# Kernel tuning notes

Measured on AMD Instinct MI355X. Metric: run time of the kernel, lower is better.

The kernel has to match this reference:

```python
import jax, jax.numpy as jnp
import numpy as np


def _scan_dir(x, A, B, reverse):
    """First-order linear recurrence h_i = A*h_{i-1} + B*x_i along last axis (W).
    x: [Bsz, C, H, W]; A, B: [C]. reverse=True scans right-to-left but returns
    states in original index order (matching torch scan_backward)."""
    xs = jnp.moveaxis(x, -1, 0)  # [W, Bsz, C, H]
    Ab = A[None, :, None]
    Bb = B[None, :, None]
    def step(h, xi):
        h = Ab * h + Bb * xi
        return h, h
    h0 = jnp.zeros_like(xs[0])
    _, hs = jax.lax.scan(step, h0, xs, reverse=reverse)
    return jnp.moveaxis(hs, 0, -1)  # [Bsz, C, H, W]


def _conv1x1(x, W, b):
    # x: [B,Cin,H,W], W: [Cout,Cin], b: [Cout]
    return jnp.einsum('bchw,dc->bdhw', x, W) + b[None, :, None, None]


def setup_inputs() -> dict:
    key = jax.random.key(0)
    ks = jax.random.split(key, 10)
    B, C, H, W = 8, 64, 128, 128
    D = 128  # hidden_dim
    return {
        'F_in': jax.random.normal(ks[0], (B, C, H, W), dtype=jnp.float32),
        'prior': jax.random.uniform(ks[1], (B, 1, H, W), dtype=jnp.float32),
        'Wi': jax.random.normal(ks[2], (D, C), dtype=jnp.float32) * 0.05,
        'bi': jnp.zeros((D,), dtype=jnp.float32),
        'A_param': jax.random.normal(ks[3], (D,), dtype=jnp.float32),
        'B_param': jax.random.normal(ks[4], (D,), dtype=jnp.float32),
        'alpha': jnp.float32(0.1),
        'gamma': jnp.float32(0.1),
        'Wf': jax.random.normal(ks[5], (D, 4 * D), dtype=jnp.float32) * 0.05,
        'bf': jnp.zeros((D,), dtype=jnp.float32),
        'Wo': jax.random.normal(ks[6], (C, D), dtype=jnp.float32) * 0.05,
        'bo': jnp.zeros((C,), dtype=jnp.float32),
    }


def reference(F_in, prior, Wi, bi, A_param, B_param, alpha, gamma, Wf, bf, Wo, bo):
    # prior has 1 channel, repeated to C channels (prior already matches HxW)
    prior_r = jnp.broadcast_to(prior, F_in.shape)
    F_mod = F_in + alpha * prior_r
    x = _conv1x1(F_mod, Wi, bi)  # [B, D, H, W]
    A = jnp.tanh(A_param)
    Bp = B_param
    h_lr = _scan_dir(x, A, Bp, reverse=False)
    h_rl = _scan_dir(x, A, Bp, reverse=True)
    xt = jnp.swapaxes(x, 2, 3)  # scan over H axis
    h_tb = jnp.swapaxes(_scan_dir(xt, A, Bp, reverse=False), 2, 3)
    h_bt = jnp.swapaxes(_scan_dir(xt, A, Bp, reverse=True), 2, 3)
    h = jnp.concatenate([h_lr, h_rl, h_tb, h_bt], axis=1)  # [B, 4D, H, W]
    h = _conv1x1(h, Wf, bf)   # fusion -> [B, D, H, W]
    out = _conv1x1(h, Wo, bo)  # output_proj -> [B, C, H, W]
    return F_mod + gamma * out
```

## Files before the change

kernel.cpp:

```cpp
#include <hip/hip_runtime.h>
#include <hip/hip_bf16.h>

typedef unsigned int u32;
typedef unsigned short u16;
typedef float f32x2 __attribute__((ext_vector_type(2)));
typedef float f32x4 __attribute__((ext_vector_type(4)));
using bf16x8 = __attribute__((ext_vector_type(8))) short;
using f32x4v = __attribute__((ext_vector_type(4))) float;

#define DEVINL __device__ __forceinline__

constexpr int LDS_AB = 65536;
constexpr int XS = 132;
constexpr int LDS_X = 128 * XS * 2;

DEVINL float bf2f(u16 u) { union { u32 i; float f; } v; v.i = ((u32)u) << 16; return v.f; }
DEVINL float bf2f_lo(u32 u) { union { u32 i; float f; } v; v.i = u << 16; return v.f; }
DEVINL float bf2f_hi(u32 u) { union { u32 i; float f; } v; v.i = u & 0xffff0000u; return v.f; }
DEVINL u16 f2bf(float f) {
  __hip_bfloat16 h = __float2bfloat16(f);
  u16 r; __builtin_memcpy(&r, &h, 2); return r;
}
DEVINL u32 pack2(float a, float b) { return (u32)f2bf(a) | ((u32)f2bf(b) << 16); }

__global__ __launch_bounds__(256) void k_pre(
    const float* __restrict__ Wf, const float* __restrict__ Wo,
    const float* __restrict__ bf_, const float* __restrict__ bo,
    const float* __restrict__ A_param, const float* __restrict__ Wi,
    float* __restrict__ A_t, float* __restrict__ beff,
    u16* __restrict__ Mrow, u16* __restrict__ Wi_bf) {
  const int wg = blockIdx.x, t = threadIdx.x;
  if (wg < 128) {
    const int idx = wg * 256 + t;
    const int cout = idx >> 9;
    const int k = idx & 511;
    float s = 0.f;
    for (int d = 0; d < 128; ++d) s = fmaf(Wo[cout * 128 + d], Wf[d * 512 + k], s);
    const int dir = k >> 7, dm = k & 127;
    Mrow[(dir * 64 + cout) * 128 + dm] = f2bf(s);
  } else if (wg == 128) {
    if (t < 128) A_t[t] = tanhf(A_param[t]);
    if (t < 64) {
      float s = bo[t];
      for (int d = 0; d < 128; ++d) s = fmaf(Wo[t * 128 + d], bf_[d], s);
      beff[t] = s;
    }
  } else {
#pragma unroll
    for (int k = 0; k < 32; ++k) {
      const int i = t + k * 256;
      Wi_bf[i] = f2bf(Wi[i]);
    }
  }
}

extern __shared__ char smem[];

template <bool REV>
DEVINL void scan_local(char* buf, int dp, int chunk, f32x2 A2) {
  f32x2 h = { 0.f, 0.f };
  const u32 cb = (u32)(dp * 4);
  const int s = chunk * 32;
  u32 nx[8];
#pragma unroll
  for (int j = 0; j < 8; ++j) {
    const int i = REV ? (127 - (s + j)) : (s + j);
    nx[j] = *(const u32*)(buf + i * 256 + (cb ^ ((u32)((i & 7) << 4))));
  }
  for (int ib = 0; ib < 32; ib += 8) {
    u32 cur[8];
#pragma unroll
    for (int j = 0; j < 8; ++j) cur[j] = nx[j];
    if (ib + 8 < 32) {
#pragma unroll
      for (int j = 0; j < 8; ++j) {
        const int i2 = s + ib + 8 + j;
        const int i = REV ? (127 - i2) : i2;
        nx[j] = *(const u32*)(buf + i * 256 + (cb ^ ((u32)((i & 7) << 4))));
      }
    }
#pragma unroll
    for (int j = 0; j < 8; ++j) {
      const int i2 = s + ib + j;
      const int i = REV ? (127 - i2) : i2;
      const f32x2 xv = { bf2f_lo(cur[j]), bf2f_hi(cur[j]) };
      h = A2 * h + xv;
      *(u32*)(buf + i * 256 + (cb ^ ((u32)((i & 7) << 4)))) = pack2(h.x, h.y);
    }
  }
}

template <bool REV>
DEVINL void scan_fix(char* buf, int dp, int chunk, f32x2 A2) {
  if (chunk == 0) return;
  f32x2 q = A2;
#pragma unroll
  for (int k = 0; k < 5; ++k) q *= q;
  const u32 cb = (u32)(dp * 4);
  f32x2 C = { 0.f, 0.f };
  for (int k = 0; k < chunk; ++k) {
    const int i2 = k * 32 + 31;
    const int i = REV ? (127 - i2) : i2;
    const u32 v = *(const u32*)(buf + i * 256 + (cb ^ ((u32)((i & 7) << 4))));
    const f32x2 xv = { bf2f_lo(v), bf2f_hi(v) };
    C = C * q + xv;
  }
  f32x2 p = A2;
  const int s = chunk * 32;
  u32 nx[8];
#pragma unroll
  for (int j = 0; j < 8; ++j) {
    const int i = REV ? (127 - (s + j)) : (s + j);
    nx[j] = *(const u32*)(buf + i * 256 + (cb ^ ((u32)((i & 7) << 4))));
  }
  for (int ib = 0; ib < 32; ib += 8) {
    u32 cur[8];
#pragma unroll
    for (int j = 0; j < 8; ++j) cur[j] = nx[j];
    if (ib + 8 < 32) {
#pragma unroll
      for (int j = 0; j < 8; ++j) {
        const int i2 = s + ib + 8 + j;
        const int i = REV ? (127 - i2) : i2;
        nx[j] = *(const u32*)(buf + i * 256 + (cb ^ ((u32)((i & 7) << 4))));
      }
    }
#pragma unroll
    for (int j = 0; j < 8; ++j) {
      const int i2 = s + ib + j;
      const int i = REV ? (127 - i2) : i2;
      const f32x2 xv = { bf2f_lo(cur[j]), bf2f_hi(cur[j]) };
      const f32x2 hv = p * C + xv;
      *(u32*)(buf + i * 256 + (cb ^ ((u32)((i & 7) << 4)))) = pack2(hv.x, hv.y);
      p *= A2;
    }
  }
}

DEVINL void run_scans512(char* bufA, char* bufB, int t, const float* __restrict__ A_t) {
  const int sub = t & 255, dp = sub & 63, chunk = sub >> 6, dir = t >> 8;
  const f32x2 a = *(const f32x2*)(A_t + dp * 2);
  char* sb = dir ? bufB : bufA;
  if (dir == 0) scan_local<false>(sb, dp, chunk, a);
  else          scan_local<true >(sb, dp, chunk, a);
  __syncthreads();
  if (dir == 0) scan_fix<false>(sb, dp, chunk, a);
  else          scan_fix<true >(sb, dp, chunk, a);
}

DEVINL void combine_full(const char* bufA, const char* bufB, const u16* __restrict__ Mrow,
                         int dir_base, int eh, int wq, int l15, int kg,
                         f32x4v (&acc2)[2][2]) {
#pragma unroll
  for (int dir = 0; dir < 2; ++dir) {
    const char* buf = dir ? bufB : bufA;
#pragma unroll
    for (int ks = 0; ks < 4; ++ks) {
      bf16x8 afr[2], bfr[2];
#pragma unroll
      for (int ct = 0; ct < 2; ++ct)
        afr[ct] = *(const bf16x8*)(Mrow + ((size_t)(dir_base + dir) * 64 + eh * 32 + ct * 16 + l15) * 128 + ks * 32 + kg * 8);
#pragma unroll
      for (int pt = 0; pt < 2; ++pt) {
        const int row = wq * 32 + pt * 16 + l15;
        bfr[pt] = *(const bf16x8*)(buf + row * 256 + ((u32)(ks * 64 + kg * 16) ^ ((u32)((row & 7) << 4))));
      }
#pragma unroll
      for (int ct = 0; ct < 2; ++ct)
#pragma unroll
        for (int pt = 0; pt < 2; ++pt)
          acc2[ct][pt] = __builtin_amdgcn_mfma_f32_16x16x32_bf16(bfr[pt], afr[ct], acc2[ct][pt], 0, 0, 0);
    }
  }
}

DEVINL void outs_epilogue512(const f32x4v (&acc2)[2][2], int eh, int wq, int l15, int kg,
                             int t, u16* __restrict__ og) {
#pragma unroll
  for (int ct = 0; ct < 2; ++ct)
#pragma unroll
    for (int pt = 0; pt < 2; ++pt) {
      const int c = eh * 32 + ct * 16 + l15;
      const int pos = wq * 32 + pt * 16 + kg * 4;
      *(f32x4v*)(smem + c * 512 + ((u32)(pos * 4) ^ ((u32)((c & 7) << 4)))) = acc2[ct][pt];
    }
  __syncthreads();
#pragma unroll
  for (int j = 0; j < 8; ++j) {
    const int i = t + j * 512;
    const int c = i >> 6, p2 = (i & 63) * 2;
    const f32x2 v = *(const f32x2*)(smem + c * 512 + ((u32)(p2 * 4) ^ ((u32)((c & 7) << 4))));
    *(u32*)(og + c * 128 + p2) = pack2(v.x, v.y);
  }
}

__global__ __launch_bounds__(512, 4) void k_A(
    const float* __restrict__ F_in, const float* __restrict__ prior,
    const u16* __restrict__ Wi_bf, const float* __restrict__ bi,
    const float* __restrict__ Bp, const float* __restrict__ alpha_p,
    const float* __restrict__ A_t, const u16* __restrict__ Mrow,
    u16* __restrict__ x2, u16* __restrict__ Shp) {
  char* bufA = smem;
  char* bufB = smem + 32768;

  const int t = threadIdx.x;
  const int lane = t & 63, wv = t >> 6;
  const int l15 = lane & 15, kg = lane >> 4;
  const int bid = blockIdx.x, b = bid >> 7, h = bid & 127;
  const int wq = wv & 3, eh = wv >> 2;

  {
    const int w = t & 127, ch = t >> 7;
    const float alpha = alpha_p[0];
    const float pv = prior[(b * 128 + h) * 128 + w];
    const float* Fb = F_in + ((size_t)b * 64 + ch * 16) * 16384 + h * 128 + w;
    const u32 sw = ((u32)((w & 7) << 4)) | (((u32)(w >> 3) & 1u) << 7);
    char* rowp = bufA + w * 256;
#pragma unroll
    for (int q = 0; q < 2; ++q) {
      float fv[8];
#pragma unroll
      for (int j = 0; j < 8; ++j) fv[j] = fmaf(alpha, pv, Fb[(q * 8 + j) * 16384]);
      uint4 pk;
      pk.x = pack2(fv[0], fv[1]); pk.y = pack2(fv[2], fv[3]);
      pk.z = pack2(fv[4], fv[5]); pk.w = pack2(fv[6], fv[7]);
      *(uint4*)(rowp + ((u32)(ch * 32 + q * 16) ^ sw)) = pk;
    }
  }
  __syncthreads();

  bf16x8 bF[2][2];
#pragma unroll
  for (int wj = 0; wj < 2; ++wj)
#pragma unroll
    for (int ks = 0; ks < 2; ++ks) {
      const int row = wq * 32 + wj * 16 + l15;
      const u32 sw = ((u32)((row & 7) << 4)) | (((u32)(row >> 3) & 1u) << 7);
      bF[wj][ks] = *(const bf16x8*)(bufA + row * 256 + ((u32)(ks * 64 + kg * 16) ^ sw));
    }
  __syncthreads();

  {
    f32x4v acc[4][2];
#pragma unroll
    for (int dt = 0; dt < 4; ++dt) {
      const f32x4 bv = *(const f32x4*)(bi + eh * 64 + dt * 16 + kg * 4);
      const f32x4v bvv = { bv.x, bv.y, bv.z, bv.w };
#pragma unroll
      for (int wj = 0; wj < 2; ++wj) acc[dt][wj] = bvv;
    }
#pragma unroll
    for (int ks = 0; ks < 2; ++ks)
#pragma unroll
      for (int dt = 0; dt < 4; ++dt) {
        const bf16x8 aWi = *(const bf16x8*)(Wi_bf + (eh * 64 + dt * 16 + l15) * 64 + ks * 32 + kg * 8);
        acc[dt][0] = __builtin_amdgcn_mfma_f32_16x16x32_bf16(aWi, bF[0][ks], acc[dt][0], 0, 0, 0);
        acc[dt][1] = __builtin_amdgcn_mfma_f32_16x16x32_bf16(aWi, bF[1][ks], acc[dt][1], 0, 0, 0);
      }
#pragma unroll
    for (int dt = 0; dt < 4; ++dt) {
      const f32x4 B4 = *(const f32x4*)(Bp + eh * 64 + dt * 16 + kg * 4);
      const f32x4v B4v = { B4.x, B4.y, B4.z, B4.w };
#pragma unroll
      for (int wj = 0; wj < 2; ++wj) {
        const f32x4v sv = acc[dt][wj] * B4v;
        const int w = wq * 32 + wj * 16 + l15;
        const int dl = eh * 64 + dt * 16 + kg * 4;
        uint2 pk;
        pk.x = pack2(sv[0], sv[1]);
        pk.y = pack2(sv[2], sv[3]);
        const u32 col = (u32)(dl * 2) ^ ((u32)((w & 7) << 4));
        *(uint2*)(bufA + w * 256 + col) = pk;
        *(uint2*)(bufB + w * 256 + col) = pk;
      }
    }
  }
  __syncthreads();

  {
    u16* xg = x2 + (size_t)bid * 16384;
#pragma unroll
    for (int j = 0; j < 4; ++j) {
      const int idx = t + j * 512;
      const int row = idx >> 4, q = idx & 15;
      const uint4 v = *(const uint4*)(bufA + row * 256 + ((u32)(q * 16) ^ ((u32)((row & 7) << 4))));
      *(uint4*)(xg + row * 128 + q * 8) = v;
    }
  }
  __syncthreads();

  run_scans512(bufA, bufB, t, A_t);
  __syncthreads();

  f32x4v acc2[2][2];
#pragma unroll
  for (int i = 0; i < 2; ++i)
#pragma unroll
    for (int j = 0; j < 2; ++j) acc2[i][j] = (f32x4v)0.f;
  combine_full(bufA, bufB, Mrow, 0, eh, wq, l15, kg, acc2);
  __syncthreads();
  outs_epilogue512(acc2, eh, wq, l15, kg, t, Shp + (size_t)bid * 8192);
}

__global__ __launch_bounds__(512, 4) void k_B(
    const u16* __restrict__ x2,
    const float* __restrict__ A_t, const u16* __restrict__ Mrow,
    u16* __restrict__ Svp) {
  char* bufA = smem;
  char* bufB = smem + 32768;

  const int t = threadIdx.x;
  const int lane = t & 63, wv = t >> 6;
  const int l15 = lane & 15, kg = lane >> 4;
  const int bid = blockIdx.x, b = bid >> 7, w = bid & 127;
  const int wq = wv & 3, eh = wv >> 2;

#pragma unroll
  for (int j = 0; j < 4; ++j) {
    const int idx = t + j * 512;
    const int hh = idx >> 4, q = idx & 15;
    const uint4 v = *(const uint4*)(x2 + ((size_t)(b * 128 + hh) * 128 + w) * 128 + q * 8);
    const u32 col = (u32)(q * 16) ^ ((u32)((hh & 7) << 4));
    *(uint4*)(bufA + hh * 256 + col) = v;
    *(uint4*)(bufB + hh * 256 + col) = v;
  }
  __syncthreads();

  run_scans512(bufA, bufB, t, A_t);
  __syncthreads();

  f32x4v acc2[2][2];
#pragma unroll
  for (int i = 0; i < 2; ++i)
#pragma unroll
    for (int j = 0; j < 2; ++j) acc2[i][j] = (f32x4v)0.f;
  combine_full(bufA, bufB, Mrow, 2, eh, wq, l15, kg, acc2);
  __syncthreads();
  outs_epilogue512(acc2, eh, wq, l15, kg, t, Svp + (size_t)bid * 8192);
}

__global__ __launch_bounds__(256) void k_final(
    const float* __restrict__ F_in, const float* __restrict__ prior,
    const float* __restrict__ alpha_p, const float* __restrict__ gamma_p,
    const float* __restrict__ beff, const u16* __restrict__ Svp,
    const u16* __restrict__ Shp, float* __restrict__ out) {
  u16* Xu = (u16*)smem;
  const int t = threadIdx.x;
  const int bid = blockIdx.x, b = bid >> 6, c = bid & 63;
  const size_t base = (size_t)bid * 16384;

  for (int i = t; i < 2048; i += 256) {
    const int w = i >> 4, q = i & 15;
    const uint4 a4 = *(const uint4*)(Svp + (size_t)(b * 128 + w) * 8192 + c * 128 + q * 8);
    u32* dst = (u32*)(Xu + w * 132 + q * 8);
    dst[0] = a4.x; dst[1] = a4.y; dst[2] = a4.z; dst[3] = a4.w;
  }
  __syncthreads();
  const float alpha = alpha_p[0], gamma = gamma_p[0];
  const float be = beff[c];
  for (int i = t; i < 2048; i += 256) {
    const int hh = i >> 4, w8 = (i & 15) * 8;
    const size_t off = base + hh * 128 + w8;
    const uint4 g0 = *(const uint4*)(Shp + (size_t)(b * 128 + hh) * 8192 + c * 128 + w8);
    const u16* p0 = (const u16*)&g0;
    const float* Fp = F_in + off;
    float* Op = out + off;
    const float* Pp = prior + (b * 128 + hh) * 128 + w8;
#pragma unroll
    for (int q = 0; q < 8; ++q) {
      const float sv = bf2f(Xu[(w8 + q) * 132 + hh]);
      Op[q] = Fp[q] + alpha * Pp[q] + gamma * (bf2f(p0[q]) + sv + be);
    }
  }
}

extern "C" void kernel_launch(void* const* d_in, const int* in_sizes, int n_in,
                              void* d_out, int out_size, void* d_ws, size_t ws_size,
                              hipStream_t stream) {
  const float* F_in   = (const float*)d_in[0];
  const float* prior  = (const float*)d_in[1];
  const float* Wi     = (const float*)d_in[2];
  const float* bi     = (const float*)d_in[3];
  const float* A_par  = (const float*)d_in[4];
  const float* B_par  = (const float*)d_in[5];
  const float* alpha  = (const float*)d_in[6];
  const float* gamma  = (const float*)d_in[7];
  const float* Wf     = (const float*)d_in[8];
  const float* bf_    = (const float*)d_in[9];
  const float* Wo     = (const float*)d_in[10];
  const float* bo     = (const float*)d_in[11];
  float* out = (float*)d_out;

  char* ws = (char*)d_ws;
  float* A_t   = (float*)ws;
  float* beff  = (float*)(ws + 512);
  u16*   Mrow  = (u16*)(ws + 1024);
  u16*   Wi_bf = (u16*)(ws + 66560);
  u16*   x2    = (u16*)(ws + 82944);
  u16*   Shp   = (u16*)(ws + 82944 + 33554432);
  u16*   Svp   = (u16*)(ws + 82944 + 67108864);

  hipFuncSetAttribute((const void*)k_A, hipFuncAttributeMaxDynamicSharedMemorySize, LDS_AB);
  hipFuncSetAttribute((const void*)k_B, hipFuncAttributeMaxDynamicSharedMemorySize, LDS_AB);

  k_pre  <<<130, 256, 0, stream>>>(Wf, Wo, bf_, bo, A_par, Wi, A_t, beff, Mrow, Wi_bf);
  k_A    <<<1024, 512, LDS_AB, stream>>>(F_in, prior, Wi_bf, bi, B_par, alpha, A_t, Mrow, x2, Shp);
  k_B    <<<1024, 512, LDS_AB, stream>>>(x2, A_t, Mrow, Svp);
  k_final<<<512, 256, LDS_X, stream>>>(F_in, prior, alpha, gamma, beff, Svp, Shp, out);
}
```

Measured before the change: 94.98 us.

## Reuse a single LDS buffer for forward and reverse scans to halve shared memory

Each scan/combine kernel previously kept two 32 KB LDS copies so the forward and backward scans could run at the same time on 512 threads. It now keeps one buffer. The forward scan runs first and its combine MFMA is applied. The forward states are then turned back into reverse-scan states in place, using a local recurrence plus a boundary value, and the second combine runs. This halves LDS per block, which should let more blocks fit per CU. The cost is that the two directions now run one after the other with only half the threads active, extra barriers are added, and the extra bf16 rounding may reduce accuracy.

```diff
diff --git a/kernel.cpp b/kernel.cpp
--- a/kernel.cpp
+++ b/kernel.cpp
@@ -10,7 +10,7 @@
 
 #define DEVINL __device__ __forceinline__
 
-constexpr int LDS_AB = 65536;
+constexpr int LDS_AB = 32768;
 constexpr int XS = 132;
 constexpr int LDS_X = 128 * XS * 2;
 
@@ -137,41 +137,95 @@
   }
 }
 
-DEVINL void run_scans512(char* bufA, char* bufB, int t, const float* __restrict__ A_t) {
-  const int sub = t & 255, dp = sub & 63, chunk = sub >> 6, dir = t >> 8;
-  const f32x2 a = *(const f32x2*)(A_t + dp * 2);
-  char* sb = dir ? bufB : bufA;
-  if (dir == 0) scan_local<false>(sb, dp, chunk, a);
-  else          scan_local<true >(sb, dp, chunk, a);
-  __syncthreads();
-  if (dir == 0) scan_fix<false>(sb, dp, chunk, a);
-  else          scan_fix<true >(sb, dp, chunk, a);
-}
-
-DEVINL void combine_full(const char* bufA, const char* bufB, const u16* __restrict__ Mrow,
-                         int dir_base, int eh, int wq, int l15, int kg,
-                         f32x4v (&acc2)[2][2]) {
-#pragma unroll
-  for (int dir = 0; dir < 2; ++dir) {
-    const char* buf = dir ? bufB : bufA;
-#pragma unroll
-    for (int ks = 0; ks < 4; ++ks) {
-      bf16x8 afr[2], bfr[2];
-#pragma unroll
-      for (int ct = 0; ct < 2; ++ct)
-        afr[ct] = *(const bf16x8*)(Mrow + ((size_t)(dir_base + dir) * 64 + eh * 32 + ct * 16 + l15) * 128 + ks * 32 + kg * 8);
-#pragma unroll
-      for (int pt = 0; pt < 2; ++pt) {
-        const int row = wq * 32 + pt * 16 + l15;
-        bfr[pt] = *(const bf16x8*)(buf + row * 256 + ((u32)(ks * 64 + kg * 16) ^ ((u32)((row & 7) << 4))));
+DEVINL void rev_convert(char* buf, int dp, int chunk, f32x2 A2, f32x2 bnd) {
+  const u32 cb = (u32)(dp * 4);
+  const int s = chunk * 32;
+  f32x2 h = { 0.f, 0.f };
+  u32 nx[8];
+#pragma unroll
+  for (int j = 0; j < 8; ++j) {
+    const int i = 127 - (s + j);
+    nx[j] = *(const u32*)(buf + i * 256 + (cb ^ ((u32)((i & 7) << 4))));
+  }
+  for (int ib = 0; ib < 32; ib += 8) {
+    u32 cur[8];
+#pragma unroll
+    for (int j = 0; j < 8; ++j) cur[j] = nx[j];
+    const bool more = (ib + 8 < 32);
+    if (more) {
+#pragma unroll
+      for (int j = 0; j < 8; ++j) {
+        const int i = 127 - (s + ib + 8 + j);
+        nx[j] = *(const u32*)(buf + i * 256 + (cb ^ ((u32)((i & 7) << 4))));
       }
-#pragma unroll
-      for (int ct = 0; ct < 2; ++ct)
-#pragma unroll
-        for (int pt = 0; pt < 2; ++pt)
-          acc2[ct][pt] = __builtin_amdgcn_mfma_f32_16x16x32_bf16(bfr[pt], afr[ct], acc2[ct][pt], 0, 0, 0);
-    }
-  }
+    }
+#pragma unroll
+    for (int j = 0; j < 8; ++j) {
+      const int i2 = s + ib + j;
+      const int i = 127 - i2;
+      const f32x2 hc = { bf2f_lo(cur[j]), bf2f_hi(cur[j]) };
+      f32x2 hn;
+      if (j < 7)     hn = (f32x2){ bf2f_lo(cur[j + 1]), bf2f_hi(cur[j + 1]) };
+      else if (more) hn = (f32x2){ bf2f_lo(nx[0]), bf2f_hi(nx[0]) };
+      else           hn = bnd;
+      const f32x2 bx = hc - A2 * hn;
+      h = A2 * h + bx;
+      *(u32*)(buf + i * 256 + (cb ^ ((u32)((i & 7) << 4)))) = pack2(h.x, h.y);
+    }
+  }
+}
+
+DEVINL void combine_one(const char* buf, const u16* __restrict__ Mrow, int dirIdx,
+                        int eh, int wq, int l15, int kg, f32x4v (&acc2)[2][2]) {
+#pragma unroll
+  for (int ks = 0; ks < 4; ++ks) {
+    bf16x8 afr[2], bfr[2];
+#pragma unroll
+    for (int ct = 0; ct < 2; ++ct)
+      afr[ct] = *(const bf16x8*)(Mrow + ((size_t)dirIdx * 64 + eh * 32 + ct * 16 + l15) * 128 + ks * 32 + kg * 8);
+#pragma unroll
+    for (int pt = 0; pt < 2; ++pt) {
+      const int row = wq * 32 + pt * 16 + l15;
+      bfr[pt] = *(const bf16x8*)(buf + row * 256 + ((u32)(ks * 64 + kg * 16) ^ ((u32)((row & 7) << 4))));
+    }
+#pragma unroll
+    for (int ct = 0; ct < 2; ++ct)
+#pragma unroll
+      for (int pt = 0; pt < 2; ++pt)
+        acc2[ct][pt] = __builtin_amdgcn_mfma_f32_16x16x32_bf16(bfr[pt], afr[ct], acc2[ct][pt], 0, 0, 0);
+  }
+}
+
+DEVINL void scan_combine_single(char* buf, int t, const float* __restrict__ A_t,
+                                const u16* __restrict__ Mrow, int dir_base,
+                                int eh, int wq, int l15, int kg, f32x4v (&acc2)[2][2]) {
+  const int dp = t & 63, chunk = (t >> 6) & 3;
+  const bool act = t < 256;
+  f32x2 a = { 0.f, 0.f };
+  if (act) a = *(const f32x2*)(A_t + dp * 2);
+
+  if (act) scan_local<false>(buf, dp, chunk, a);
+  __syncthreads();
+  if (act) scan_fix<false>(buf, dp, chunk, a);
+  __syncthreads();
+
+  combine_one(buf, Mrow, dir_base, eh, wq, l15, kg, acc2);
+  __syncthreads();
+
+  f32x2 bnd = { 0.f, 0.f };
+  if (act && chunk < 3) {
+    const int i = 127 - (chunk * 32 + 32);
+    const u32 v = *(const u32*)(buf + i * 256 + ((u32)(dp * 4) ^ ((u32)((i & 7) << 4))));
+    bnd = (f32x2){ bf2f_lo(v), bf2f_hi(v) };
+  }
+  __syncthreads();
+  if (act) rev_convert(buf, dp, chunk, a, bnd);
+  __syncthreads();
+  if (act) scan_fix<true>(buf, dp, chunk, a);
+  __syncthreads();
+
+  combine_one(buf, Mrow, dir_base + 1, eh, wq, l15, kg, acc2);
+  __syncthreads();
 }
 
 DEVINL void outs_epilogue512(const f32x4v (&acc2)[2][2], int eh, int wq, int l15, int kg,
@@ -200,8 +254,7 @@
     const float* __restrict__ Bp, const float* __restrict__ alpha_p,
     const float* __restrict__ A_t, const u16* __restrict__ Mrow,
     u16* __restrict__ x2, u16* __restrict__ Shp) {
-  char* bufA = smem;
-  char* bufB = smem + 32768;
+  char* buf = smem;
 
   const int t = threadIdx.x;
   const int lane = t & 63, wv = t >> 6;
@@ -215,7 +268,7 @@
     const float pv = prior[(b * 128 + h) * 128 + w];
     const float* Fb = F_in + ((size_t)b * 64 + ch * 16) * 16384 + h * 128 + w;
     const u32 sw = ((u32)((w & 7) << 4)) | (((u32)(w >> 3) & 1u) << 7);
-    char* rowp = bufA + w * 256;
+    char* rowp = buf + w * 256;
 #pragma unroll
     for (int q = 0; q < 2; ++q) {
       float fv[8];
@@ -236,7 +289,7 @@
     for (int ks = 0; ks < 2; ++ks) {
       const int row = wq * 32 + wj * 16 + l15;
       const u32 sw = ((u32)((row & 7) << 4)) | (((u32)(row >> 3) & 1u) << 7);
-      bF[wj][ks] = *(const bf16x8*)(bufA + row * 256 + ((u32)(ks * 64 + kg * 16) ^ sw));
+      bF[wj][ks] = *(const bf16x8*)(buf + row * 256 + ((u32)(ks * 64 + kg * 16) ^ sw));
     }
   __syncthreads();
 
@@ -270,8 +323,7 @@
         pk.x = pack2(sv[0], sv[1]);
         pk.y = pack2(sv[2], sv[3]);
         const u32 col = (u32)(dl * 2) ^ ((u32)((w & 7) << 4));
-        *(uint2*)(bufA + w * 256 + col) = pk;
-        *(uint2*)(bufB + w * 256 + col) = pk;
+        *(uint2*)(buf + w * 256 + col) = pk;
       }
     }
   }
@@ -283,22 +335,19 @@
     for (int j = 0; j < 4; ++j) {
       const int idx = t + j * 512;
       const int row = idx >> 4, q = idx & 15;
-      const uint4 v = *(const uint4*)(bufA + row * 256 + ((u32)(q * 16) ^ ((u32)((row & 7) << 4))));
+      const uint4 v = *(const uint4*)(buf + row * 256 + ((u32)(q * 16) ^ ((u32)((row & 7) << 4))));
       *(uint4*)(xg + row * 128 + q * 8) = v;
     }
   }
   __syncthreads();
 
-  run_scans512(bufA, bufB, t, A_t);
-  __syncthreads();
-
   f32x4v acc2[2][2];
 #pragma unroll
   for (int i = 0; i < 2; ++i)
 #pragma unroll
     for (int j = 0; j < 2; ++j) acc2[i][j] = (f32x4v)0.f;
-  combine_full(bufA, bufB, Mrow, 0, eh, wq, l15, kg, acc2);
-  __syncthreads();
+  scan_combine_single(buf, t, A_t, Mrow, 0, eh, wq, l15, kg, acc2);
+
   outs_epilogue512(acc2, eh, wq, l15, kg, t, Shp + (size_t)bid * 8192);
 }
 
@@ -306,8 +355,7 @@
     const u16* __restrict__ x2,
     const float* __restrict__ A_t, const u16* __restrict__ Mrow,
     u16* __restrict__ Svp) {
-  char* bufA = smem;
-  char* bufB = smem + 32768;
+  char* buf = smem;
 
   const int t = threadIdx.x;
   const int lane = t & 63, wv = t >> 6;
@@ -321,12 +369,8 @@
     const int hh = idx >> 4, q = idx & 15;
     const uint4 v = *(const uint4*)(x2 + ((size_t)(b * 128 + hh) * 128 + w) * 128 + q * 8);
     const u32 col = (u32)(q * 16) ^ ((u32)((hh & 7) << 4));
-    *(uint4*)(bufA + hh * 256 + col) = v;
-    *(uint4*)(bufB + hh * 256 + col) = v;
-  }
-  __syncthreads();
-
-  run_scans512(bufA, bufB, t, A_t);
+    *(uint4*)(buf + hh * 256 + col) = v;
+  }
   __syncthreads();
 
   f32x4v acc2[2][2];
@@ -334,8 +378,8 @@
   for (int i = 0; i < 2; ++i)
 #pragma unroll
     for (int j = 0; j < 2; ++j) acc2[i][j] = (f32x4v)0.f;
-  combine_full(bufA, bufB, Mrow, 2, eh, wq, l15, kg, acc2);
-  __syncthreads();
+  scan_combine_single(buf, t, A_t, Mrow, 2, eh, wq, l15, kg, acc2);
+
   outs_epilogue512(acc2, eh, wq, l15, kg, t, Svp + (size_t)bid * 8192);
 }
 
```

Measured after the change: 101.5 us. 6.8% more time.
